# Optimization experiments

Measured on AMD Instinct MI355X. Metric: run time of the kernel, lower is better.

Reference implementation:

```python
import jax, jax.numpy as jnp
import numpy as np

B, MAXF, NFEAT, FT_OUT = 16384, 32, 768, 1024

def setup_inputs() -> dict:
    key = jax.random.key(0)
    k1, k2, k3, k4, k5, k6 = jax.random.split(key, 6)
    values = jnp.ones((B, MAXF), dtype=jnp.float32)
    stm_indices = jax.random.randint(k1, (B, MAXF), 0, NFEAT, dtype=jnp.int32)
    nstm_indices = jax.random.randint(k2, (B, MAXF), 0, NFEAT, dtype=jnp.int32)
    ft_w = jax.random.normal(k3, (NFEAT, FT_OUT), dtype=jnp.float32) * 0.02
    ft_b = jax.random.normal(k4, (FT_OUT,), dtype=jnp.float32) * 0.02
    out_w = jax.random.normal(k5, (2 * FT_OUT, 1), dtype=jnp.float32) * 0.02
    out_b = jax.random.normal(k6, (1,), dtype=jnp.float32) * 0.02
    return {"values": values, "stm_indices": stm_indices, "nstm_indices": nstm_indices,
            "ft_w": ft_w, "ft_b": ft_b, "out_w": out_w, "out_b": out_b}

def _ft_slice(indices, values, ft_w, ft_b):
    # sparse gather-accumulate: [B, MAXF] indices into [NFEAT, FT_OUT] table
    gathered = jnp.take(ft_w, indices, axis=0)          # [B, MAXF, FT_OUT]
    return jnp.einsum('bf,bfd->bd', values, gathered) + ft_b  # [B, FT_OUT]

def reference(values, stm_indices, nstm_indices, ft_w, ft_b, out_w, out_b):
    stm_ft = _ft_slice(stm_indices, values, ft_w, ft_b)
    nstm_ft = _ft_slice(nstm_indices, values, ft_w, ft_b)
    hidden = jnp.clip(jnp.concatenate([stm_ft, nstm_ft], axis=1), 0.0, 1.0)
    return jax.nn.sigmoid(hidden @ out_w + out_b)  # [B, 1]
```

## Files before the change

### kernel.cpp

```cpp
#include <hip/hip_runtime.h>
#include <hip/hip_fp16.h>
#include <math.h>

#define BATCH 16384
#define MAXF 32
#define NFEAT 768
#define FT_OUT 1024
#define CHUNK 32
#define NCHUNK (FT_OUT / CHUNK)
#define GROUPS 24
#define CH_HALVES (NFEAT * CHUNK)

#define GET4(a, f) (((f) & 3) == 0 ? (a)[(f) >> 2].x : \
                    ((f) & 3) == 1 ? (a)[(f) >> 2].y : \
                    ((f) & 3) == 2 ? (a)[(f) >> 2].z : (a)[(f) >> 2].w)

typedef unsigned int uint_t;

__global__ __launch_bounds__(256, 3) void nnboard_main(
    const float* __restrict__ values,
    const int*   __restrict__ stm_idx,
    const int*   __restrict__ nstm_idx,
    const float* __restrict__ ft_w,
    const float* __restrict__ ft_b,
    const float* __restrict__ out_w,
    float*       __restrict__ partials)
{
    __shared__ __half s_tab[CH_HALVES];

    const int tid = threadIdx.x;
    const int c = blockIdx.x % NCHUNK;
    const int g = blockIdx.x / NCHUNK;
    const __half2 zero2 = __float2half2_rn(0.f);

    {
        const int lane8 = tid & 7;
        const int rbase = tid >> 3;
        #pragma unroll
        for (int k = 0; k < NFEAT / 32; ++k) {
            const int r = k * 32 + rbase;
            const float4 f = *(const float4*)(ft_w + (size_t)r * FT_OUT + c * CHUNK + lane8 * 4);
            __half2 h0 = __floats2half2_rn(f.x, f.y);
            __half2 h1 = __floats2half2_rn(f.z, f.w);
            uint2 u;
            u.x = *reinterpret_cast<uint_t*>(&h0);
            u.y = *reinterpret_cast<uint_t*>(&h1);
            *(uint2*)(s_tab + r * CHUNK + lane8 * 4) = u;
        }
    }
    __syncthreads();

    const int grp = tid >> 2;
    const int j   = tid & 3;
    const int col0 = c * CHUNK + j * 8;
    const __half* my_tab = s_tab + j * 8;

    const float4 bia0 = *(const float4*)(ft_b + col0);
    const float4 bia1 = *(const float4*)(ft_b + col0 + 4);
    const float4 ws0  = *(const float4*)(out_w + col0);
    const float4 ws1  = *(const float4*)(out_w + col0 + 4);
    const float4 wn0  = *(const float4*)(out_w + FT_OUT + col0);
    const float4 wn1  = *(const float4*)(out_w + FT_OUT + col0 + 4);

    for (int it = g; it < BATCH / 64; it += GROUPS) {
        const int b = it * 64 + grp;

        const int4*   sp = (const int4*)(stm_idx + b * MAXF);
        const int4*   np = (const int4*)(nstm_idx + b * MAXF);
        const float4* vp = (const float4*)(values + b * MAXF);
        int4 si[8], ni[8];
        float4 vv[8];
        #pragma unroll
        for (int k = 0; k < 8; ++k) { si[k] = sp[k]; ni[k] = np[k]; vv[k] = vp[k]; }

        __half2 accs[4] = {zero2, zero2, zero2, zero2};
        __half2 accn[4] = {zero2, zero2, zero2, zero2};

        #pragma unroll
        for (int f = 0; f < MAXF; ++f) {
            const int is = GET4(si, f);
            const int in = GET4(ni, f);
            const __half2 v2 = __float2half2_rn(GET4(vv, f));
            const uint4 qs = *(const uint4*)(my_tab + is * CHUNK);
            const uint4 qn = *(const uint4*)(my_tab + in * CHUNK);
            accs[0] = __hfma2(*(const __half2*)&qs.x, v2, accs[0]);
            accs[1] = __hfma2(*(const __half2*)&qs.y, v2, accs[1]);
            accs[2] = __hfma2(*(const __half2*)&qs.z, v2, accs[2]);
            accs[3] = __hfma2(*(const __half2*)&qs.w, v2, accs[3]);
            accn[0] = __hfma2(*(const __half2*)&qn.x, v2, accn[0]);
            accn[1] = __hfma2(*(const __half2*)&qn.y, v2, accn[1]);
            accn[2] = __hfma2(*(const __half2*)&qn.z, v2, accn[2]);
            accn[3] = __hfma2(*(const __half2*)&qn.w, v2, accn[3]);
        }

        float p = 0.f;
        {
            const float2 f0 = __half22float2(accs[0]);
            const float2 f1 = __half22float2(accs[1]);
            const float2 f2 = __half22float2(accs[2]);
            const float2 f3 = __half22float2(accs[3]);
            const float2 g0 = __half22float2(accn[0]);
            const float2 g1 = __half22float2(accn[1]);
            const float2 g2 = __half22float2(accn[2]);
            const float2 g3 = __half22float2(accn[3]);
            auto clip = [](float x) { return fminf(fmaxf(x, 0.f), 1.f); };
            p = fmaf(clip(f0.x + bia0.x), ws0.x, p);
            p = fmaf(clip(f0.y + bia0.y), ws0.y, p);
            p = fmaf(clip(f1.x + bia0.z), ws0.z, p);
            p = fmaf(clip(f1.y + bia0.w), ws0.w, p);
            p = fmaf(clip(f2.x + bia1.x), ws1.x, p);
            p = fmaf(clip(f2.y + bia1.y), ws1.y, p);
            p = fmaf(clip(f3.x + bia1.z), ws1.z, p);
            p = fmaf(clip(f3.y + bia1.w), ws1.w, p);
            p = fmaf(clip(g0.x + bia0.x), wn0.x, p);
            p = fmaf(clip(g0.y + bia0.y), wn0.y, p);
            p = fmaf(clip(g1.x + bia0.z), wn0.z, p);
            p = fmaf(clip(g1.y + bia0.w), wn0.w, p);
            p = fmaf(clip(g2.x + bia1.x), wn1.x, p);
            p = fmaf(clip(g2.y + bia1.y), wn1.y, p);
            p = fmaf(clip(g3.x + bia1.z), wn1.z, p);
            p = fmaf(clip(g3.y + bia1.w), wn1.w, p);
        }

        p += __shfl_down(p, 1, 64);
        p += __shfl_down(p, 2, 64);
        if (j == 0) partials[c * BATCH + b] = p;
    }
}

__global__ __launch_bounds__(256) void reduce_sigmoid_kernel(
    const float* __restrict__ partials,
    const float* __restrict__ out_b,
    float* __restrict__ out)
{
    const int i = blockIdx.x * 256 + threadIdx.x;
    float s = out_b[0];
    #pragma unroll
    for (int k = 0; k < NCHUNK; ++k)
        s += partials[k * BATCH + i];
    out[i] = 1.f / (1.f + expf(-s));
}

extern "C" void kernel_launch(void* const* d_in, const int* in_sizes, int n_in,
                              void* d_out, int out_size, void* d_ws, size_t ws_size,
                              hipStream_t stream) {
    const float* values   = (const float*)d_in[0];
    const int*   stm_idx  = (const int*)d_in[1];
    const int*   nstm_idx = (const int*)d_in[2];
    const float* ft_w     = (const float*)d_in[3];
    const float* ft_b     = (const float*)d_in[4];
    const float* out_w    = (const float*)d_in[5];
    const float* out_b    = (const float*)d_in[6];
    float*       out      = (float*)d_out;

    float* partials = (float*)d_ws;

    nnboard_main<<<NCHUNK * GROUPS, 256, 0, stream>>>(
        values, stm_idx, nstm_idx, ft_w, ft_b, out_w, partials);
    reduce_sigmoid_kernel<<<BATCH / 256, 256, 0, stream>>>(partials, out_b, out);
}
```

Before: 110.3 us.

## Widen LDS table chunk to 64 columns to halve index re-reads

Doubles the per-block column chunk of the fp16 feature table held in LDS from 32 to 64 columns, so each block stores a 96KB table in dynamic shared memory. There are now half as many chunks, so the index and value rows are read from global memory half as often and the partials buffer has half the chunk rows. Each batch row is handled by 8 threads with an extra shuffle step, and the grid shrinks to 256 blocks. The cost is occupancy: launch bounds drop to one block per CU, and the larger LDS tile makes each block's table load longer.

```diff
diff --git a/kernel.cpp b/kernel.cpp
--- a/kernel.cpp
+++ b/kernel.cpp
@@ -6,10 +6,11 @@
 #define MAXF 32
 #define NFEAT 768
 #define FT_OUT 1024
-#define CHUNK 32
+#define CHUNK 64
 #define NCHUNK (FT_OUT / CHUNK)
-#define GROUPS 24
+#define GROUPS 16
 #define CH_HALVES (NFEAT * CHUNK)
+#define LDS_BYTES (CH_HALVES * 2)
 
 #define GET4(a, f) (((f) & 3) == 0 ? (a)[(f) >> 2].x : \
                     ((f) & 3) == 1 ? (a)[(f) >> 2].y : \
@@ -17,7 +18,7 @@
 
 typedef unsigned int uint_t;
 
-__global__ __launch_bounds__(256, 3) void nnboard_main(
+__global__ __launch_bounds__(256, 1) void nnboard_main(
     const float* __restrict__ values,
     const int*   __restrict__ stm_idx,
     const int*   __restrict__ nstm_idx,
@@ -26,11 +27,11 @@
     const float* __restrict__ out_w,
     float*       __restrict__ partials)
 {
-    __shared__ __half s_tab[CH_HALVES];
+    extern __shared__ __half s_tab[];
 
     const int tid = threadIdx.x;
-    const int c = blockIdx.x % NCHUNK;
-    const int g = blockIdx.x / NCHUNK;
+    const int c = blockIdx.x & (NCHUNK - 1);
+    const int g = blockIdx.x >> 4;
     const __half2 zero2 = __float2half2_rn(0.f);
 
     {
@@ -39,21 +40,27 @@
         #pragma unroll
         for (int k = 0; k < NFEAT / 32; ++k) {
             const int r = k * 32 + rbase;
-            const float4 f = *(const float4*)(ft_w + (size_t)r * FT_OUT + c * CHUNK + lane8 * 4);
-            __half2 h0 = __floats2half2_rn(f.x, f.y);
-            __half2 h1 = __floats2half2_rn(f.z, f.w);
-            uint2 u;
+            const float* src = ft_w + (size_t)r * FT_OUT + c * CHUNK + lane8 * 8;
+            const float4 f0 = *(const float4*)(src);
+            const float4 f1 = *(const float4*)(src + 4);
+            __half2 h0 = __floats2half2_rn(f0.x, f0.y);
+            __half2 h1 = __floats2half2_rn(f0.z, f0.w);
+            __half2 h2 = __floats2half2_rn(f1.x, f1.y);
+            __half2 h3 = __floats2half2_rn(f1.z, f1.w);
+            uint4 u;
             u.x = *reinterpret_cast<uint_t*>(&h0);
             u.y = *reinterpret_cast<uint_t*>(&h1);
-            *(uint2*)(s_tab + r * CHUNK + lane8 * 4) = u;
+            u.z = *reinterpret_cast<uint_t*>(&h2);
+            u.w = *reinterpret_cast<uint_t*>(&h3);
+            *(uint4*)(s_tab + r * CHUNK + lane8 * 8) = u;
         }
     }
     __syncthreads();
 
-    const int grp = tid >> 2;
-    const int j   = tid & 3;
-    const int col0 = c * CHUNK + j * 8;
-    const __half* my_tab = s_tab + j * 8;
+    const int grp = tid >> 3;
+    const int jj  = tid & 7;
+    const int col0 = c * CHUNK + jj * 8;
+    const __half* my_tab = s_tab + jj * 8;
 
     const float4 bia0 = *(const float4*)(ft_b + col0);
     const float4 bia1 = *(const float4*)(ft_b + col0 + 4);
@@ -62,8 +69,8 @@
     const float4 wn0  = *(const float4*)(out_w + FT_OUT + col0);
     const float4 wn1  = *(const float4*)(out_w + FT_OUT + col0 + 4);
 
-    for (int it = g; it < BATCH / 64; it += GROUPS) {
-        const int b = it * 64 + grp;
+    for (int it = g; it < BATCH / 32; it += GROUPS) {
+        const int b = it * 32 + grp;
 
         const int4*   sp = (const int4*)(stm_idx + b * MAXF);
         const int4*   np = (const int4*)(nstm_idx + b * MAXF);
@@ -124,7 +131,8 @@
 
         p += __shfl_down(p, 1, 64);
         p += __shfl_down(p, 2, 64);
-        if (j == 0) partials[c * BATCH + b] = p;
+        p += __shfl_down(p, 4, 64);
+        if (jj == 0) partials[c * BATCH + b] = p;
     }
 }
 
@@ -155,7 +163,10 @@
 
     float* partials = (float*)d_ws;
 
-    nnboard_main<<<NCHUNK * GROUPS, 256, 0, stream>>>(
+    hipFuncSetAttribute((const void*)nnboard_main,
+                        hipFuncAttributeMaxDynamicSharedMemorySize, LDS_BYTES);
+
+    nnboard_main<<<NCHUNK * GROUPS, 256, LDS_BYTES, stream>>>(
         values, stm_idx, nstm_idx, ft_w, ft_b, out_w, partials);
     reduce_sigmoid_kernel<<<BATCH / 256, 256, 0, stream>>>(partials, out_b, out);
 }
```

Measured after the change: 188.3 us. 1.71x slower.
